# Kernel optimization log

Measured on AMD Instinct MI355X. Metric: run time of the kernel, lower is better.

Reference implementation:

```python
import jax, jax.numpy as jnp
import numpy as np

B, NA, NB = 2, 2048, 2048
DIM_A, DIM_B = 256, 256
HEADS, DH_A, DH_B = 8, 64, 64
INNER_A, INNER_B = DH_A * HEADS, DH_B * HEADS
EPS = 1e-5


def layer_norm(x, w, b):
    m = jnp.mean(x, axis=-1, keepdims=True)
    v = jnp.mean(jnp.square(x - m), axis=-1, keepdims=True)
    return (x - m) * jax.lax.rsqrt(v + EPS) * w + b


def setup_inputs() -> dict:
    key = jax.random.key(0)
    ks = jax.random.split(key, 16)
    s = 0.02
    return {
        "feat_a": jax.random.normal(ks[0], (B, NA, DIM_A), jnp.float32),
        "feat_b": jax.random.normal(ks[1], (B, NB, DIM_B), jnp.float32),
        "mask_a_b": jax.random.bernoulli(ks[2], 0.5, (B, NA, NB)),
        # linear weights stored (in, out)
        "Wq": jax.random.normal(ks[3], (DIM_A, INNER_B), jnp.float32) * s,
        "bq": jnp.zeros((INNER_B,), jnp.float32),
        "Wk": jax.random.normal(ks[4], (DIM_B, INNER_B), jnp.float32) * s,
        "bk": jnp.zeros((INNER_B,), jnp.float32),
        "Wv": jax.random.normal(ks[5], (DIM_B, INNER_A), jnp.float32) * s,
        "bv": jnp.zeros((INNER_A,), jnp.float32),
        "Wg": jax.random.normal(ks[6], (DIM_A, INNER_A), jnp.float32) * s,
        "bg": jnp.zeros((INNER_A,), jnp.float32),
        "Wo": jax.random.normal(ks[7], (INNER_A, DIM_A), jnp.float32) * s,
        "bo": jnp.zeros((DIM_A,), jnp.float32),
        "ln_a_w": jnp.ones((DIM_A,), jnp.float32),
        "ln_a_b": jnp.zeros((DIM_A,), jnp.float32),
        "ln_b_w": jnp.ones((DIM_B,), jnp.float32),
        "ln_b_b": jnp.zeros((DIM_B,), jnp.float32),
        "qln_w": jnp.ones((INNER_B,), jnp.float32),
        "qln_b": jnp.zeros((INNER_B,), jnp.float32),
        "kln_w": jnp.ones((INNER_B,), jnp.float32),
        "kln_b": jnp.zeros((INNER_B,), jnp.float32),
    }


def reference(feat_a, feat_b, mask_a_b, Wq, bq, Wk, bk, Wv, bv, Wg, bg, Wo, bo,
              ln_a_w, ln_a_b, ln_b_w, ln_b_b, qln_w, qln_b, kln_w, kln_b):
    scale = DH_B ** -0.5
    fa = layer_norm(feat_a, ln_a_w, ln_a_b)            # (b, na, dim_a)
    fb = layer_norm(feat_b, ln_b_w, ln_b_b)            # (b, nb, dim_b)
    q = layer_norm(fa @ Wq + bq, qln_w, qln_b)         # (b, na, inner_b)
    k = layer_norm(fb @ Wk + bk, kln_w, kln_b)         # (b, nb, inner_b)
    v = fb @ Wv + bv                                   # (b, nb, inner_a)
    g = fa @ Wg + bg                                   # (b, na, inner_a)
    q = q.reshape(B, NA, HEADS, DH_B)
    k = k.reshape(B, NB, HEADS, DH_B)
    v = v.reshape(B, NB, HEADS, DH_A)
    g = g.reshape(B, NA, HEADS, DH_A)
    sim = jnp.einsum('bihd,bjhd->bhij', q, k) * scale  # (b, h, na, nb)
    neg = jnp.finfo(sim.dtype).min
    sim = jnp.where(mask_a_b[:, None, :, :], sim, neg)
    attn = jax.nn.softmax(sim, axis=-1)
    out = jnp.einsum('bhij,bjhd->bihd', attn, v)       # (b, na, h, dh_a)
    out = jax.nn.sigmoid(g) * out
    out = out.reshape(B, NA, INNER_A)
    return out @ Wo + bo                               # (b, na, dim_a)
```

## Files before the change

kernel.cpp:

```cpp
#include <hip/hip_runtime.h>
#include <hip/hip_bf16.h>

using bf16 = __hip_bfloat16;
typedef short bf16x8 __attribute__((ext_vector_type(8)));
typedef float f32x4 __attribute__((ext_vector_type(4)));
typedef unsigned long long u64;

static constexpr int NA_ = 2048, NB_ = 2048;
static constexpr int H_ = 8, DH_ = 64, INNER_ = 512;
static constexpr int MROWS = 2 * NA_;

__device__ __forceinline__ unsigned short bfbits(float x) {
  bf16 h = __float2bfloat16(x);
  return __builtin_bit_cast(unsigned short, h);
}

__device__ __forceinline__ float exp2_fast(float x) {
#if __has_builtin(__builtin_amdgcn_exp2f)
  return __builtin_amdgcn_exp2f(x);
#else
  return exp2f(x);
#endif
}

__global__ __launch_bounds__(256) void ln_feat_kernel(
    const float* __restrict__ fa_in, const float* __restrict__ fb_in,
    const float* __restrict__ law, const float* __restrict__ lab,
    const float* __restrict__ lbw, const float* __restrict__ lbb,
    bf16* __restrict__ fa, bf16* __restrict__ fb) {
  int row = blockIdx.x;
  const float *src, *w, *bb;
  bf16* dst;
  int r;
  if (row < MROWS) { src = fa_in; w = law; bb = lab; dst = fa; r = row; }
  else             { src = fb_in; w = lbw; bb = lbb; dst = fb; r = row - MROWS; }
  int t = threadIdx.x;
  float x = src[(size_t)r * 256 + t];
  float s = x, s2 = x * x;
#pragma unroll
  for (int m = 32; m >= 1; m >>= 1) { s += __shfl_xor(s, m); s2 += __shfl_xor(s2, m); }
  __shared__ float red[8];
  if ((t & 63) == 0) { red[t >> 6] = s; red[(t >> 6) + 4] = s2; }
  __syncthreads();
  float ts  = red[0] + red[1] + red[2] + red[3];
  float ts2 = red[4] + red[5] + red[6] + red[7];
  float mean = ts * (1.0f / 256.0f);
  float var  = ts2 * (1.0f / 256.0f) - mean * mean;
  float rstd = rsqrtf(var + 1e-5f);
  dst[(size_t)r * 256 + t] = __float2bfloat16((x - mean) * rstd * w[t] + bb[t]);
}

__global__ __launch_bounds__(256) void wconv_kernel(
    const float* __restrict__ Wq, const float* __restrict__ Wk,
    const float* __restrict__ Wv, const float* __restrict__ Wg,
    const float* __restrict__ Wo,
    bf16* __restrict__ Wqgt, bf16* __restrict__ Wkvt,
    bf16* __restrict__ Woth, bf16* __restrict__ Wotl) {
  int z = blockIdx.z;
  int idx = blockIdx.x * 256 + threadIdx.x;
  if (z < 4) {
    const float* W = (z == 0) ? Wq : (z == 1) ? Wk : (z == 2) ? Wv : Wg;
    bf16* Wt = (z == 0 || z == 3) ? Wqgt : Wkvt;
    int half = (z == 2 || z == 3) ? 512 : 0;
    int kk = idx >> 9, n = idx & 511;
    Wt[(half + n) * 256 + kk] = __float2bfloat16(W[idx]);
  } else {
    int kk = idx >> 8, n = idx & 255;
    float w = Wo[idx];
    bf16 hi = __float2bfloat16(w);
    Woth[n * 512 + kk] = hi;
    Wotl[n * 512 + kk] = __float2bfloat16(w - __bfloat162float(hi));
  }
}

__global__ void maskdetect_kernel(const unsigned char* __restrict__ m, int* __restrict__ flag) {
  int t = threadIdx.x;
  if (t == 0) *flag = 0;
  __syncthreads();
  if ((t & 3) != 0 && m[t] != 0) atomicOr(flag, 1);
}

__global__ __launch_bounds__(256) void maskpack_kernel(
    const void* __restrict__ maskp, const int* __restrict__ mflag,
    u64* __restrict__ mbits) {
  const bool m8 = (*mflag != 0);
  int lane = threadIdx.x & 63;
  int wid = threadIdx.x >> 6;
  const size_t NW = 131072;
  for (size_t word = (size_t)blockIdx.x * 4 + wid; word < NW; word += (size_t)gridDim.x * 4) {
    size_t e = word * 64 + lane;
    int v = m8 ? (int)((const unsigned char*)maskp)[e] : ((const int*)maskp)[e];
    u64 bal = __ballot(v != 0);
    if (lane == 0) mbits[word] = bal;
  }
}

template <int VARIANT>
__global__ __launch_bounds__(256) void gemm_fused_kernel(
    const bf16* __restrict__ A, const bf16* __restrict__ Wt,
    const float* __restrict__ bias1, const float* __restrict__ bias2,
    float* __restrict__ C1, bf16* __restrict__ C2) {
  constexpr int K = 256;
  __shared__ __align__(16) bf16 As[64 * 72];
  __shared__ __align__(16) bf16 Bs[64 * 72];
  int n0 = blockIdx.x * 64, m0 = blockIdx.y * 64;
  int t = threadIdx.x, wave = t >> 6, lane = t & 63;
  int lm = lane & 15, quad = lane >> 4, q8 = quad * 8;
  int wm = (wave & 1) * 32, wn = (wave >> 1) * 32;
  f32x4 acc[2][2] = {};
  for (int k0 = 0; k0 < K; k0 += 64) {
    __syncthreads();
#pragma unroll
    for (int i = 0; i < 4; i++) {
      int id = t + 256 * i, r = id >> 4, c = id & 15;
      *(ushort4*)(&As[r * 72 + c * 4]) =
          *(const ushort4*)(A + (size_t)(m0 + r) * K + k0 + c * 4);
      *(ushort4*)(&Bs[r * 72 + c * 4]) =
          *(const ushort4*)(Wt + (size_t)(n0 + r) * K + k0 + c * 4);
    }
    __syncthreads();
#pragma unroll
    for (int kk = 0; kk < 64; kk += 32) {
      bf16x8 af[2], bf_[2];
#pragma unroll
      for (int i = 0; i < 2; i++) {
        af[i]  = *(const bf16x8*)(&As[(wm + i * 16 + lm) * 72 + kk + q8]);
        bf_[i] = *(const bf16x8*)(&Bs[(wn + i * 16 + lm) * 72 + kk + q8]);
      }
#pragma unroll
      for (int mi = 0; mi < 2; mi++)
#pragma unroll
        for (int ni = 0; ni < 2; ni++)
          acc[mi][ni] = __builtin_amdgcn_mfma_f32_16x16x32_bf16(af[mi], bf_[ni], acc[mi][ni], 0, 0, 0);
    }
  }
  if (n0 < 512) {
#pragma unroll
    for (int mi = 0; mi < 2; mi++)
#pragma unroll
      for (int ni = 0; ni < 2; ni++) {
        int n = n0 + wn + ni * 16 + lm;
        float bvv = bias1[n];
        int mb = m0 + wm + mi * 16 + quad * 4;
#pragma unroll
        for (int r = 0; r < 4; r++) C1[(size_t)(mb + r) * 512 + n] = acc[mi][ni][r] + bvv;
      }
  } else if (VARIANT == 0) {
#pragma unroll
    for (int mi = 0; mi < 2; mi++)
#pragma unroll
      for (int ni = 0; ni < 2; ni++) {
        int nn = n0 - 512 + wn + ni * 16 + lm;
        float bvv = bias2[nn];
        int mb = m0 + wm + mi * 16 + quad * 4;
#pragma unroll
        for (int r = 0; r < 4; r++)
          C2[(size_t)(mb + r) * 512 + nn] = __float2bfloat16(acc[mi][ni][r] + bvv);
      }
  } else {
    __syncthreads();
#pragma unroll
    for (int mi = 0; mi < 2; mi++)
#pragma unroll
      for (int ni = 0; ni < 2; ni++) {
        int d_local = wn + ni * 16 + lm;
        float bvv = bias2[n0 - 512 + d_local];
        int j_local = wm + mi * 16 + quad * 4;
#pragma unroll
        for (int r = 0; r < 4; r++)
          As[d_local * 72 + j_local + r] = __float2bfloat16(acc[mi][ni][r] + bvv);
      }
    __syncthreads();
    int bidx = m0 >> 11, j0g = m0 & 2047;
    int hh = (n0 - 512) >> 6;
    int dl = t >> 2, jc = (t & 3) * 16;
    bf16* dstrow = C2 + (size_t)((bidx * 8 + hh) * 64 + dl) * 2048 + j0g + jc;
#pragma unroll
    for (int c = 0; c < 4; c++)
      *(ushort4*)(dstrow + c * 4) = *(const ushort4*)(&As[dl * 72 + jc + c * 4]);
  }
}

__global__ __launch_bounds__(256) void qkln_kernel(
    const float* __restrict__ qpre, const float* __restrict__ kpre,
    const float* __restrict__ qw, const float* __restrict__ qb,
    const float* __restrict__ kw, const float* __restrict__ kb,
    bf16* __restrict__ qo, bf16* __restrict__ ko) {
  int row = blockIdx.x;
  const float *src, *w, *bb;
  bf16* dst;
  int r;
  if (row < MROWS) { src = qpre; w = qw; bb = qb; dst = qo; r = row; }
  else             { src = kpre; w = kw; bb = kb; dst = ko; r = row - MROWS; }
  int t = threadIdx.x;
  float x0 = src[(size_t)r * 512 + t];
  float x1 = src[(size_t)r * 512 + 256 + t];
  float s = x0 + x1, s2 = x0 * x0 + x1 * x1;
#pragma unroll
  for (int m = 32; m >= 1; m >>= 1) { s += __shfl_xor(s, m); s2 += __shfl_xor(s2, m); }
  __shared__ float red[8];
  if ((t & 63) == 0) { red[t >> 6] = s; red[(t >> 6) + 4] = s2; }
  __syncthreads();
  float ts  = red[0] + red[1] + red[2] + red[3];
  float ts2 = red[4] + red[5] + red[6] + red[7];
  float mean = ts * (1.0f / 512.0f);
  float var  = ts2 * (1.0f / 512.0f) - mean * mean;
  float rstd = rsqrtf(var + 1e-5f);
  dst[(size_t)r * 512 + t]       = __float2bfloat16((x0 - mean) * rstd * w[t] + bb[t]);
  dst[(size_t)r * 512 + 256 + t] = __float2bfloat16((x1 - mean) * rstd * w[256 + t] + bb[256 + t]);
}

__global__ __launch_bounds__(512) void attn_kernel(
    const bf16* __restrict__ q, const bf16* __restrict__ k,
    const bf16* __restrict__ vt, const bf16* __restrict__ g,
    const u64* __restrict__ mbits,
    bf16* __restrict__ gh, bf16* __restrict__ gl) {
  __shared__ __align__(16) char smem[65024];
  bf16* Qs = (bf16*)smem;
  bf16* KsB = (bf16*)(smem + 9216);
  bf16* VsB = (bf16*)(smem + 27648);
  bf16* PsB = (bf16*)(smem + 46080);
  float* Om = (float*)(smem + 9216);
  float* Lbuf = (float*)(smem + 64512);

  int qt = blockIdx.x, bh = blockIdx.y;
  int bidx = bh >> 3, h = bh & 7;
  int i0 = qt * 64;
  int t = threadIdx.x, wave = t >> 6, lane = t & 63;
  int jhalf = wave >> 2, w4 = wave & 3;
  int lm = lane & 15, quad = lane >> 4, q8 = quad * 8;
  int lt = t & 255;

#pragma unroll
  for (int i = 0; i < 2; i++) {
    int id = t + 512 * i, r = id >> 4, c = id & 15;
    *(ushort4*)(&Qs[r * 72 + c * 4]) =
        *(const ushort4*)(q + (size_t)(bidx * NA_ + i0 + r) * INNER_ + h * DH_ + c * 4);
  }
  __syncthreads();
  bf16x8 bq[2];
  bq[0] = *(const bf16x8*)(&Qs[(w4 * 16 + lm) * 72 + q8]);
  bq[1] = *(const bf16x8*)(&Qs[(w4 * 16 + lm) * 72 + 32 + q8]);

  f32x4 oacc[4] = {};
  float psum = 0.f;
  const float scale2 = 0.125f * 1.44269504088896f;

  const bf16* kb = k + (size_t)(bidx * NB_) * INNER_ + h * DH_;
  const bf16* vb = vt + (size_t)(bh * DH_) * NB_;
  bf16* Pw = PsB + wave * (16 * 72);
  bf16* Ks = KsB + jhalf * (64 * 72);
  bf16* Vs = VsB + jhalf * (64 * 72);
  const u64* mrp = mbits + ((size_t)(bidx * NA_ + i0 + w4 * 16 + lm)) * (NB_ / 64) + jhalf * 16;

  for (int it = 0; it < 16; it++) {
    int j0 = jhalf * 1024 + it * 64;
    __syncthreads();
#pragma unroll
    for (int i = 0; i < 4; i++) {
      int id = lt + 256 * i, r = id >> 4, c = id & 15;
      *(ushort4*)(&Ks[r * 72 + c * 4]) =
          *(const ushort4*)(kb + (size_t)(j0 + r) * INNER_ + c * 4);
      *(ushort4*)(&Vs[r * 72 + c * 4]) =
          *(const ushort4*)(vb + (size_t)r * NB_ + j0 + c * 4);
    }
    u64 sm = mrp[it] >> (quad * 4);
    __syncthreads();

    f32x4 st[4];
#pragma unroll
    for (int nt = 0; nt < 4; nt++) {
      bf16x8 a0 = *(const bf16x8*)(&Ks[(nt * 16 + lm) * 72 + q8]);
      bf16x8 a1 = *(const bf16x8*)(&Ks[(nt * 16 + lm) * 72 + 32 + q8]);
      f32x4 a = {0.f, 0.f, 0.f, 0.f};
      a = __builtin_amdgcn_mfma_f32_16x16x32_bf16(a0, bq[0], a, 0, 0, 0);
      a = __builtin_amdgcn_mfma_f32_16x16x32_bf16(a1, bq[1], a, 0, 0, 0);
      st[nt] = a;
    }

    float pr[4][4];
#pragma unroll
    for (int nt = 0; nt < 4; nt++)
#pragma unroll
      for (int r = 0; r < 4; r++) {
        float p = exp2_fast(st[nt][r] * scale2 - 16.0f);
        unsigned live = (unsigned)(sm >> (nt * 16 + r)) & 1u;
        pr[nt][r] = live ? p : 0.0f;
      }

    float s0 = (pr[0][0] + pr[0][1]) + (pr[0][2] + pr[0][3]);
    float s1 = (pr[1][0] + pr[1][1]) + (pr[1][2] + pr[1][3]);
    float s2 = (pr[2][0] + pr[2][1]) + (pr[2][2] + pr[2][3]);
    float s3 = (pr[3][0] + pr[3][1]) + (pr[3][2] + pr[3][3]);
    psum += (s0 + s1) + (s2 + s3);

#pragma unroll
    for (int nt = 0; nt < 4; nt++) {
      ushort4 pk;
      pk.x = bfbits(pr[nt][0]);
      pk.y = bfbits(pr[nt][1]);
      pk.z = bfbits(pr[nt][2]);
      pk.w = bfbits(pr[nt][3]);
      *(ushort4*)(Pw + lm * 72 + nt * 16 + quad * 4) = pk;
    }

    bf16x8 ap0 = *(const bf16x8*)(&Pw[lm * 72 + q8]);
    bf16x8 ap1 = *(const bf16x8*)(&Pw[lm * 72 + 32 + q8]);
#pragma unroll
    for (int c = 0; c < 4; c++) {
      bf16x8 v0 = *(const bf16x8*)(&Vs[(c * 16 + lm) * 72 + q8]);
      bf16x8 v1 = *(const bf16x8*)(&Vs[(c * 16 + lm) * 72 + 32 + q8]);
      oacc[c] = __builtin_amdgcn_mfma_f32_16x16x32_bf16(ap0, v0, oacc[c], 0, 0, 0);
      oacc[c] = __builtin_amdgcn_mfma_f32_16x16x32_bf16(ap1, v1, oacc[c], 0, 0, 0);
    }
  }

  psum += __shfl_xor(psum, 16);
  psum += __shfl_xor(psum, 32);

  __syncthreads();
  if (quad == 0) Lbuf[jhalf * 64 + w4 * 16 + lm] = psum;
  if (jhalf == 1) {
#pragma unroll
    for (int c = 0; c < 4; c++)
#pragma unroll
      for (int r = 0; r < 4; r++)
        Om[w4 * (16 * 66) + (quad * 4 + r) * 66 + c * 16 + lm] = oacc[c][r];
  }
  __syncthreads();
  if (jhalf == 0) {
    int mrow = i0 + w4 * 16 + quad * 4;
    float inv[4];
#pragma unroll
    for (int r = 0; r < 4; r++) {
      float l = Lbuf[w4 * 16 + quad * 4 + r] + Lbuf[64 + w4 * 16 + quad * 4 + r];
      inv[r] = 1.0f / l;
    }
#pragma unroll
    for (int c = 0; c < 4; c++) {
      int col = h * DH_ + c * 16 + lm;
#pragma unroll
      for (int r = 0; r < 4; r++) {
        float o = oacc[c][r] + Om[w4 * (16 * 66) + (quad * 4 + r) * 66 + c * 16 + lm];
        size_t idx = (size_t)(bidx * NA_ + mrow + r) * INNER_ + col;
        float gv = __bfloat162float(g[idx]);
        float sig = 1.0f / (1.0f + __expf(-gv));
        float val = o * inv[r] * sig;
        bf16 hi = __float2bfloat16(val);
        gh[idx] = hi;
        gl[idx] = __float2bfloat16(val - __bfloat162float(hi));
      }
    }
  }
}

__global__ __launch_bounds__(256) void gemm_split_kernel(
    const bf16* __restrict__ Ah, const bf16* __restrict__ Al,
    const bf16* __restrict__ Bh, const bf16* __restrict__ Bl,
    const float* __restrict__ bias, float* __restrict__ C,
    int M, int N, int K) {
  __shared__ __align__(16) bf16 Ash[64 * 72];
  __shared__ __align__(16) bf16 Asl[64 * 72];
  __shared__ __align__(16) bf16 Bsh[64 * 72];
  __shared__ __align__(16) bf16 Bsl[64 * 72];
  int n0 = blockIdx.x * 64, m0 = blockIdx.y * 64;
  int t = threadIdx.x, wave = t >> 6, lane = t & 63;
  int lm = lane & 15, quad = lane >> 4, q8 = quad * 8;
  int wm = (wave & 1) * 32, wn = (wave >> 1) * 32;
  f32x4 acc[2][2] = {};
  for (int k0 = 0; k0 < K; k0 += 64) {
    __syncthreads();
#pragma unroll
    for (int i = 0; i < 4; i++) {
      int id = t + 256 * i, r = id >> 4, c = id & 15;
      size_t ga = (size_t)(m0 + r) * K + k0 + c * 4;
      size_t gb = (size_t)(n0 + r) * K + k0 + c * 4;
      *(ushort4*)(&Ash[r * 72 + c * 4]) = *(const ushort4*)(Ah + ga);
      *(ushort4*)(&Asl[r * 72 + c * 4]) = *(const ushort4*)(Al + ga);
      *(ushort4*)(&Bsh[r * 72 + c * 4]) = *(const ushort4*)(Bh + gb);
      *(ushort4*)(&Bsl[r * 72 + c * 4]) = *(const ushort4*)(Bl + gb);
    }
    __syncthreads();
#pragma unroll
    for (int kk = 0; kk < 64; kk += 32) {
      bf16x8 ah[2], al[2], bh[2], bl[2];
#pragma unroll
      for (int i = 0; i < 2; i++) {
        ah[i] = *(const bf16x8*)(&Ash[(wm + i * 16 + lm) * 72 + kk + q8]);
        al[i] = *(const bf16x8*)(&Asl[(wm + i * 16 + lm) * 72 + kk + q8]);
        bh[i] = *(const bf16x8*)(&Bsh[(wn + i * 16 + lm) * 72 + kk + q8]);
        bl[i] = *(const bf16x8*)(&Bsl[(wn + i * 16 + lm) * 72 + kk + q8]);
      }
#pragma unroll
      for (int mi = 0; mi < 2; mi++)
#pragma unroll
        for (int ni = 0; ni < 2; ni++) {
          acc[mi][ni] = __builtin_amdgcn_mfma_f32_16x16x32_bf16(ah[mi], bh[ni], acc[mi][ni], 0, 0, 0);
          acc[mi][ni] = __builtin_amdgcn_mfma_f32_16x16x32_bf16(ah[mi], bl[ni], acc[mi][ni], 0, 0, 0);
          acc[mi][ni] = __builtin_amdgcn_mfma_f32_16x16x32_bf16(al[mi], bh[ni], acc[mi][ni], 0, 0, 0);
        }
    }
  }
#pragma unroll
  for (int mi = 0; mi < 2; mi++)
#pragma unroll
    for (int ni = 0; ni < 2; ni++) {
      int n = n0 + wn + ni * 16 + lm;
      float bvv = bias[n];
      int mb = m0 + wm + mi * 16 + quad * 4;
#pragma unroll
      for (int r = 0; r < 4; r++) C[(size_t)(mb + r) * N + n] = acc[mi][ni][r] + bvv;
    }
}

extern "C" void kernel_launch(void* const* d_in, const int* in_sizes, int n_in,
                              void* d_out, int out_size, void* d_ws, size_t ws_size,
                              hipStream_t stream) {
  const float* feat_a = (const float*)d_in[0];
  const float* feat_b = (const float*)d_in[1];
  const void*  mask   = d_in[2];
  const float* Wq = (const float*)d_in[3];
  const float* bq = (const float*)d_in[4];
  const float* Wk = (const float*)d_in[5];
  const float* bk = (const float*)d_in[6];
  const float* Wv = (const float*)d_in[7];
  const float* bv = (const float*)d_in[8];
  const float* Wg = (const float*)d_in[9];
  const float* bg = (const float*)d_in[10];
  const float* Wo = (const float*)d_in[11];
  const float* bo = (const float*)d_in[12];
  const float* law = (const float*)d_in[13];
  const float* lab = (const float*)d_in[14];
  const float* lbw = (const float*)d_in[15];
  const float* lbb = (const float*)d_in[16];
  const float* qlw = (const float*)d_in[17];
  const float* qlb = (const float*)d_in[18];
  const float* klw = (const float*)d_in[19];
  const float* klb = (const float*)d_in[20];

  char* ws = (char*)d_ws;
  size_t off = 0;
  auto alloc = [&](size_t bytes) -> void* {
    void* p = ws + off;
    off += (bytes + 255) & ~(size_t)255;
    return p;
  };
  bf16* fa    = (bf16*)alloc((size_t)MROWS * 256 * 2);
  bf16* fb    = (bf16*)alloc((size_t)MROWS * 256 * 2);
  bf16* Wqgt  = (bf16*)alloc((size_t)1024 * 256 * 2);
  bf16* Wkvt  = (bf16*)alloc((size_t)1024 * 256 * 2);
  bf16* Woth  = (bf16*)alloc((size_t)131072 * 2);
  bf16* Wotl  = (bf16*)alloc((size_t)131072 * 2);
  float* qpre = (float*)alloc((size_t)MROWS * 512 * 4);
  float* kpre = (float*)alloc((size_t)MROWS * 512 * 4);
  bf16* qb_   = (bf16*)alloc((size_t)MROWS * 512 * 2);
  bf16* kb_   = (bf16*)alloc((size_t)MROWS * 512 * 2);
  bf16* vtb   = (bf16*)alloc((size_t)1024 * 2048 * 2);
  bf16* gbuf  = (bf16*)alloc((size_t)MROWS * 512 * 2);
  bf16* gh    = (bf16*)alloc((size_t)MROWS * 512 * 2);
  bf16* gl    = (bf16*)alloc((size_t)MROWS * 512 * 2);
  u64*  mbits = (u64*)alloc((size_t)131072 * 8);
  int*  mflag = (int*)alloc(256);

  ln_feat_kernel<<<2 * MROWS, 256, 0, stream>>>(feat_a, feat_b, law, lab, lbw, lbb, fa, fb);
  wconv_kernel<<<dim3(512, 1, 5), 256, 0, stream>>>(Wq, Wk, Wv, Wg, Wo, Wqgt, Wkvt, Woth, Wotl);
  maskdetect_kernel<<<1, 256, 0, stream>>>((const unsigned char*)mask, mflag);
  maskpack_kernel<<<2048, 256, 0, stream>>>(mask, mflag, mbits);
  gemm_fused_kernel<0><<<dim3(16, 64), 256, 0, stream>>>(fa, Wqgt, bq, bg, qpre, gbuf);
  gemm_fused_kernel<1><<<dim3(16, 64), 256, 0, stream>>>(fb, Wkvt, bk, bv, kpre, vtb);
  qkln_kernel<<<2 * MROWS, 256, 0, stream>>>(qpre, kpre, qlw, qlb, klw, klb, qb_, kb_);
  attn_kernel<<<dim3(32, 16), 512, 0, stream>>>(qb_, kb_, vtb, gbuf, mbits, gh, gl);
  gemm_split_kernel<<<dim3(4, 64), 256, 0, stream>>>(gh, gl, Woth, Wotl, bo, (float*)d_out, MROWS, 256, 512);
}
```

Baseline: 213.9 us.

## Fuse Q/K projection with LayerNorm and restructure attention and pipeline kernels

Merges the Q/K projection GEMM with its LayerNorm in one kernel, so the fp32 qpre/kpre intermediates and the separate qkln pass go away. G/V projection moves into its own GEMM kernel. The attention kernel now uses 256 threads, each wave covering all key blocks in 128-column tiles, which removes the cross-half partial-output merge through shared memory; it can also use 16x16x16 MFMA with P held in registers. Loads are widened to 16 bytes throughout, the feature LayerNorm packs one row per wave, and the output GEMM uses smaller M tiles for more blocks. The risks are lower occupancy per attention block and longer serial loops per wave.

```diff
diff --git a/kernel.cpp b/kernel.cpp
--- a/kernel.cpp
+++ b/kernel.cpp
@@ -3,24 +3,34 @@
 
 using bf16 = __hip_bfloat16;
 typedef short bf16x8 __attribute__((ext_vector_type(8)));
+typedef short bf16x4 __attribute__((ext_vector_type(4)));
 typedef float f32x4 __attribute__((ext_vector_type(4)));
+typedef unsigned short ushort8_t __attribute__((ext_vector_type(8)));
 typedef unsigned long long u64;
 
 static constexpr int NA_ = 2048, NB_ = 2048;
 static constexpr int H_ = 8, DH_ = 64, INNER_ = 512;
 static constexpr int MROWS = 2 * NA_;
 
+#define MFMA32(a, b, c) __builtin_amdgcn_mfma_f32_16x16x32_bf16(a, b, c, 0, 0, 0)
+
+#if __has_builtin(__builtin_amdgcn_mfma_f32_16x16x16bf16_1k)
+#define HAS_MFMA16 1
+#define MFMA16(a, b, c) __builtin_amdgcn_mfma_f32_16x16x16bf16_1k(a, b, c, 0, 0, 0)
+#elif __has_builtin(__builtin_amdgcn_mfma_f32_16x16x16_bf16)
+#define HAS_MFMA16 1
+#define MFMA16(a, b, c) __builtin_amdgcn_mfma_f32_16x16x16_bf16(a, b, c, 0, 0, 0)
+#else
+#define HAS_MFMA16 0
+#endif
+
 __device__ __forceinline__ unsigned short bfbits(float x) {
   bf16 h = __float2bfloat16(x);
   return __builtin_bit_cast(unsigned short, h);
 }
-
-__device__ __forceinline__ float exp2_fast(float x) {
-#if __has_builtin(__builtin_amdgcn_exp2f)
-  return __builtin_amdgcn_exp2f(x);
-#else
-  return exp2f(x);
-#endif
+__device__ __forceinline__ float b2f(unsigned short u) {
+  unsigned v = ((unsigned)u) << 16;
+  return __builtin_bit_cast(float, v);
 }
 
 __global__ __launch_bounds__(256) void ln_feat_kernel(
@@ -28,42 +38,45 @@
     const float* __restrict__ law, const float* __restrict__ lab,
     const float* __restrict__ lbw, const float* __restrict__ lbb,
     bf16* __restrict__ fa, bf16* __restrict__ fb) {
-  int row = blockIdx.x;
+  int row = blockIdx.x * 4 + (threadIdx.x >> 6);
+  int lane = threadIdx.x & 63;
   const float *src, *w, *bb;
   bf16* dst;
   int r;
   if (row < MROWS) { src = fa_in; w = law; bb = lab; dst = fa; r = row; }
   else             { src = fb_in; w = lbw; bb = lbb; dst = fb; r = row - MROWS; }
-  int t = threadIdx.x;
-  float x = src[(size_t)r * 256 + t];
-  float s = x, s2 = x * x;
+  float4 x = *(const float4*)(src + (size_t)r * 256 + lane * 4);
+  float s  = (x.x + x.y) + (x.z + x.w);
+  float s2 = (x.x * x.x + x.y * x.y) + (x.z * x.z + x.w * x.w);
 #pragma unroll
   for (int m = 32; m >= 1; m >>= 1) { s += __shfl_xor(s, m); s2 += __shfl_xor(s2, m); }
-  __shared__ float red[8];
-  if ((t & 63) == 0) { red[t >> 6] = s; red[(t >> 6) + 4] = s2; }
-  __syncthreads();
-  float ts  = red[0] + red[1] + red[2] + red[3];
-  float ts2 = red[4] + red[5] + red[6] + red[7];
-  float mean = ts * (1.0f / 256.0f);
-  float var  = ts2 * (1.0f / 256.0f) - mean * mean;
+  float mean = s * (1.0f / 256.0f);
+  float var  = s2 * (1.0f / 256.0f) - mean * mean;
   float rstd = rsqrtf(var + 1e-5f);
-  dst[(size_t)r * 256 + t] = __float2bfloat16((x - mean) * rstd * w[t] + bb[t]);
+  float4 wv = *(const float4*)(w + lane * 4);
+  float4 bv = *(const float4*)(bb + lane * 4);
+  ushort4 o;
+  o.x = bfbits((x.x - mean) * rstd * wv.x + bv.x);
+  o.y = bfbits((x.y - mean) * rstd * wv.y + bv.y);
+  o.z = bfbits((x.z - mean) * rstd * wv.z + bv.z);
+  o.w = bfbits((x.w - mean) * rstd * wv.w + bv.w);
+  *(ushort4*)(dst + (size_t)r * 256 + lane * 4) = o;
 }
 
 __global__ __launch_bounds__(256) void wconv_kernel(
     const float* __restrict__ Wq, const float* __restrict__ Wk,
     const float* __restrict__ Wv, const float* __restrict__ Wg,
     const float* __restrict__ Wo,
-    bf16* __restrict__ Wqgt, bf16* __restrict__ Wkvt,
+    bf16* __restrict__ Wqt, bf16* __restrict__ Wkt,
+    bf16* __restrict__ Wvt, bf16* __restrict__ Wgt,
     bf16* __restrict__ Woth, bf16* __restrict__ Wotl) {
   int z = blockIdx.z;
   int idx = blockIdx.x * 256 + threadIdx.x;
   if (z < 4) {
     const float* W = (z == 0) ? Wq : (z == 1) ? Wk : (z == 2) ? Wv : Wg;
-    bf16* Wt = (z == 0 || z == 3) ? Wqgt : Wkvt;
-    int half = (z == 2 || z == 3) ? 512 : 0;
+    bf16* Wt = (z == 0) ? Wqt : (z == 1) ? Wkt : (z == 2) ? Wvt : Wgt;
     int kk = idx >> 9, n = idx & 511;
-    Wt[(half + n) * 256 + kk] = __float2bfloat16(W[idx]);
+    Wt[n * 256 + kk] = __float2bfloat16(W[idx]);
   } else {
     int kk = idx >> 8, n = idx & 255;
     float w = Wo[idx];
@@ -95,14 +108,117 @@
   }
 }
 
-template <int VARIANT>
-__global__ __launch_bounds__(256) void gemm_fused_kernel(
-    const bf16* __restrict__ A, const bf16* __restrict__ Wt,
-    const float* __restrict__ bias1, const float* __restrict__ bias2,
-    float* __restrict__ C1, bf16* __restrict__ C2) {
+__global__ __launch_bounds__(512) void qk_ln_gemm_kernel(
+    const bf16* __restrict__ fa, const bf16* __restrict__ fb,
+    const bf16* __restrict__ Wqt, const bf16* __restrict__ Wkt,
+    const float* __restrict__ bq, const float* __restrict__ bk,
+    const float* __restrict__ qlw, const float* __restrict__ qlb,
+    const float* __restrict__ klw, const float* __restrict__ klb,
+    bf16* __restrict__ qo, bf16* __restrict__ ko) {
+  __shared__ __align__(16) bf16 As[32 * 264];
+  __shared__ float Pred[32 * 16];
+  __shared__ float MV[64];
+  int z = blockIdx.y;
+  const bf16* A    = z ? fb : fa;
+  const bf16* Wt   = z ? Wkt : Wqt;
+  const float* bias = z ? bk : bq;
+  const float* lw  = z ? klw : qlw;
+  const float* lb  = z ? klb : qlb;
+  bf16* out        = z ? ko : qo;
+  int m0 = blockIdx.x * 32;
+  int t = threadIdx.x, wave = t >> 6, lane = t & 63;
+  int lm = lane & 15, quad = lane >> 4, q8 = quad * 8;
+  int n0w = wave * 64;
+#pragma unroll
+  for (int i = 0; i < 2; i++) {
+    int id = t + 512 * i, r = id >> 5, cg = id & 31;
+    *(ushort8_t*)(&As[r * 264 + cg * 8]) =
+        *(const ushort8_t*)(A + (size_t)(m0 + r) * 256 + cg * 8);
+  }
+  __syncthreads();
+  f32x4 acc[2][4] = {};
+  const bf16* wrow[4];
+#pragma unroll
+  for (int ni = 0; ni < 4; ni++) wrow[ni] = Wt + (size_t)(n0w + ni * 16 + lm) * 256;
+#pragma unroll
+  for (int ks = 0; ks < 8; ks++) {
+    int k0 = ks * 32;
+    bf16x8 bf_[4], af[2];
+#pragma unroll
+    for (int ni = 0; ni < 4; ni++) bf_[ni] = *(const bf16x8*)(wrow[ni] + k0 + q8);
+#pragma unroll
+    for (int mi = 0; mi < 2; mi++)
+      af[mi] = *(const bf16x8*)(&As[(mi * 16 + lm) * 264 + k0 + q8]);
+#pragma unroll
+    for (int mi = 0; mi < 2; mi++)
+#pragma unroll
+      for (int ni = 0; ni < 4; ni++)
+        acc[mi][ni] = MFMA32(af[mi], bf_[ni], acc[mi][ni]);
+  }
+  float bv[4];
+#pragma unroll
+  for (int ni = 0; ni < 4; ni++) bv[ni] = bias[n0w + ni * 16 + lm];
+#pragma unroll
+  for (int mi = 0; mi < 2; mi++)
+#pragma unroll
+    for (int ni = 0; ni < 4; ni++)
+#pragma unroll
+      for (int r = 0; r < 4; r++) acc[mi][ni][r] += bv[ni];
+#pragma unroll
+  for (int mi = 0; mi < 2; mi++)
+#pragma unroll
+    for (int r = 0; r < 4; r++) {
+      float s  = (acc[mi][0][r] + acc[mi][1][r]) + (acc[mi][2][r] + acc[mi][3][r]);
+      float s2 = (acc[mi][0][r] * acc[mi][0][r] + acc[mi][1][r] * acc[mi][1][r]) +
+                 (acc[mi][2][r] * acc[mi][2][r] + acc[mi][3][r] * acc[mi][3][r]);
+#pragma unroll
+      for (int m = 1; m <= 8; m <<= 1) { s += __shfl_xor(s, m); s2 += __shfl_xor(s2, m); }
+      if (lm == 0) {
+        int row = mi * 16 + quad * 4 + r;
+        Pred[row * 16 + wave * 2]     = s;
+        Pred[row * 16 + wave * 2 + 1] = s2;
+      }
+    }
+  __syncthreads();
+  if (t < 32) {
+    float s = 0.f, s2 = 0.f;
+#pragma unroll
+    for (int w = 0; w < 8; w++) { s += Pred[t * 16 + w * 2]; s2 += Pred[t * 16 + w * 2 + 1]; }
+    float mean = s * (1.0f / 512.0f);
+    float var  = s2 * (1.0f / 512.0f) - mean * mean;
+    MV[t * 2]     = mean;
+    MV[t * 2 + 1] = rsqrtf(var + 1e-5f);
+  }
+  __syncthreads();
+  float lww[4], lbb_[4];
+#pragma unroll
+  for (int ni = 0; ni < 4; ni++) { lww[ni] = lw[n0w + ni * 16 + lm]; lbb_[ni] = lb[n0w + ni * 16 + lm]; }
+#pragma unroll
+  for (int mi = 0; mi < 2; mi++)
+#pragma unroll
+    for (int r = 0; r < 4; r++) {
+      int row = mi * 16 + quad * 4 + r;
+      float mean = MV[row * 2], rstd = MV[row * 2 + 1];
+      size_t obase = (size_t)(m0 + row) * 512 + n0w;
+#pragma unroll
+      for (int ni = 0; ni < 4; ni++)
+        out[obase + ni * 16 + lm] =
+            __float2bfloat16((acc[mi][ni][r] - mean) * rstd * lww[ni] + lbb_[ni]);
+    }
+}
+
+__global__ __launch_bounds__(256) void gv_gemm_kernel(
+    const bf16* __restrict__ fa, const bf16* __restrict__ fb,
+    const bf16* __restrict__ Wgt, const bf16* __restrict__ Wvt,
+    const float* __restrict__ bg, const float* __restrict__ bv,
+    bf16* __restrict__ gout, bf16* __restrict__ vout) {
   constexpr int K = 256;
   __shared__ __align__(16) bf16 As[64 * 72];
   __shared__ __align__(16) bf16 Bs[64 * 72];
+  int z = blockIdx.z;
+  const bf16* A    = z ? fb : fa;
+  const bf16* Wt   = z ? Wvt : Wgt;
+  const float* bias = z ? bv : bg;
   int n0 = blockIdx.x * 64, m0 = blockIdx.y * 64;
   int t = threadIdx.x, wave = t >> 6, lane = t & 63;
   int lm = lane & 15, quad = lane >> 4, q8 = quad * 8;
@@ -111,12 +227,12 @@
   for (int k0 = 0; k0 < K; k0 += 64) {
     __syncthreads();
 #pragma unroll
-    for (int i = 0; i < 4; i++) {
-      int id = t + 256 * i, r = id >> 4, c = id & 15;
-      *(ushort4*)(&As[r * 72 + c * 4]) =
-          *(const ushort4*)(A + (size_t)(m0 + r) * K + k0 + c * 4);
-      *(ushort4*)(&Bs[r * 72 + c * 4]) =
-          *(const ushort4*)(Wt + (size_t)(n0 + r) * K + k0 + c * 4);
+    for (int i = 0; i < 2; i++) {
+      int id = t + 256 * i, r = id >> 3, cg = id & 7;
+      *(ushort8_t*)(&As[r * 72 + cg * 8]) =
+          *(const ushort8_t*)(A + (size_t)(m0 + r) * K + k0 + cg * 8);
+      *(ushort8_t*)(&Bs[r * 72 + cg * 8]) =
+          *(const ushort8_t*)(Wt + (size_t)(n0 + r) * K + k0 + cg * 8);
     }
     __syncthreads();
 #pragma unroll
@@ -131,31 +247,20 @@
       for (int mi = 0; mi < 2; mi++)
 #pragma unroll
         for (int ni = 0; ni < 2; ni++)
-          acc[mi][ni] = __builtin_amdgcn_mfma_f32_16x16x32_bf16(af[mi], bf_[ni], acc[mi][ni], 0, 0, 0);
-    }
-  }
-  if (n0 < 512) {
+          acc[mi][ni] = MFMA32(af[mi], bf_[ni], acc[mi][ni]);
+    }
+  }
+  if (z == 0) {
 #pragma unroll
     for (int mi = 0; mi < 2; mi++)
 #pragma unroll
       for (int ni = 0; ni < 2; ni++) {
-        int n = n0 + wn + ni * 16 + lm;
-        float bvv = bias1[n];
+        int nn = n0 + wn + ni * 16 + lm;
+        float bvv = bias[nn];
         int mb = m0 + wm + mi * 16 + quad * 4;
 #pragma unroll
-        for (int r = 0; r < 4; r++) C1[(size_t)(mb + r) * 512 + n] = acc[mi][ni][r] + bvv;
-      }
-  } else if (VARIANT == 0) {
-#pragma unroll
-    for (int mi = 0; mi < 2; mi++)
-#pragma unroll
-      for (int ni = 0; ni < 2; ni++) {
-        int nn = n0 - 512 + wn + ni * 16 + lm;
-        float bvv = bias2[nn];
-        int mb = m0 + wm + mi * 16 + quad * 4;
-#pragma unroll
         for (int r = 0; r < 4; r++)
-          C2[(size_t)(mb + r) * 512 + nn] = __float2bfloat16(acc[mi][ni][r] + bvv);
+          gout[(size_t)(mb + r) * 512 + nn] = __float2bfloat16(acc[mi][ni][r] + bvv);
       }
   } else {
     __syncthreads();
@@ -164,7 +269,7 @@
 #pragma unroll
       for (int ni = 0; ni < 2; ni++) {
         int d_local = wn + ni * 16 + lm;
-        float bvv = bias2[n0 - 512 + d_local];
+        float bvv = bias[n0 + d_local];
         int j_local = wm + mi * 16 + quad * 4;
 #pragma unroll
         for (int r = 0; r < 4; r++)
@@ -172,245 +277,204 @@
       }
     __syncthreads();
     int bidx = m0 >> 11, j0g = m0 & 2047;
-    int hh = (n0 - 512) >> 6;
+    int hh = n0 >> 6;
     int dl = t >> 2, jc = (t & 3) * 16;
-    bf16* dstrow = C2 + (size_t)((bidx * 8 + hh) * 64 + dl) * 2048 + j0g + jc;
+    bf16* dstrow = vout + (size_t)((bidx * 8 + hh) * 64 + dl) * 2048 + j0g + jc;
 #pragma unroll
     for (int c = 0; c < 4; c++)
       *(ushort4*)(dstrow + c * 4) = *(const ushort4*)(&As[dl * 72 + jc + c * 4]);
   }
 }
 
-__global__ __launch_bounds__(256) void qkln_kernel(
-    const float* __restrict__ qpre, const float* __restrict__ kpre,
-    const float* __restrict__ qw, const float* __restrict__ qb,
-    const float* __restrict__ kw, const float* __restrict__ kb,
-    bf16* __restrict__ qo, bf16* __restrict__ ko) {
-  int row = blockIdx.x;
-  const float *src, *w, *bb;
-  bf16* dst;
-  int r;
-  if (row < MROWS) { src = qpre; w = qw; bb = qb; dst = qo; r = row; }
-  else             { src = kpre; w = kw; bb = kb; dst = ko; r = row - MROWS; }
-  int t = threadIdx.x;
-  float x0 = src[(size_t)r * 512 + t];
-  float x1 = src[(size_t)r * 512 + 256 + t];
-  float s = x0 + x1, s2 = x0 * x0 + x1 * x1;
-#pragma unroll
-  for (int m = 32; m >= 1; m >>= 1) { s += __shfl_xor(s, m); s2 += __shfl_xor(s2, m); }
-  __shared__ float red[8];
-  if ((t & 63) == 0) { red[t >> 6] = s; red[(t >> 6) + 4] = s2; }
-  __syncthreads();
-  float ts  = red[0] + red[1] + red[2] + red[3];
-  float ts2 = red[4] + red[5] + red[6] + red[7];
-  float mean = ts * (1.0f / 512.0f);
-  float var  = ts2 * (1.0f / 512.0f) - mean * mean;
-  float rstd = rsqrtf(var + 1e-5f);
-  dst[(size_t)r * 512 + t]       = __float2bfloat16((x0 - mean) * rstd * w[t] + bb[t]);
-  dst[(size_t)r * 512 + 256 + t] = __float2bfloat16((x1 - mean) * rstd * w[256 + t] + bb[256 + t]);
-}
-
-__global__ __launch_bounds__(512) void attn_kernel(
+__global__ __launch_bounds__(256) void attn_kernel(
     const bf16* __restrict__ q, const bf16* __restrict__ k,
     const bf16* __restrict__ vt, const bf16* __restrict__ g,
     const u64* __restrict__ mbits,
     bf16* __restrict__ gh, bf16* __restrict__ gl) {
-  __shared__ __align__(16) char smem[65024];
+  __shared__ __align__(16) char smem[45056];
   bf16* Qs = (bf16*)smem;
-  bf16* KsB = (bf16*)(smem + 9216);
-  bf16* VsB = (bf16*)(smem + 27648);
-  bf16* PsB = (bf16*)(smem + 46080);
-  float* Om = (float*)(smem + 9216);
-  float* Lbuf = (float*)(smem + 64512);
-
+  bf16* Ks = (bf16*)(smem + 9216);
+  bf16* Vs = (bf16*)(smem + 27648);
+#if !HAS_MFMA16
+  __shared__ __align__(16) bf16 Ps[4][16 * 136];
+#endif
   int qt = blockIdx.x, bh = blockIdx.y;
   int bidx = bh >> 3, h = bh & 7;
   int i0 = qt * 64;
   int t = threadIdx.x, wave = t >> 6, lane = t & 63;
-  int jhalf = wave >> 2, w4 = wave & 3;
   int lm = lane & 15, quad = lane >> 4, q8 = quad * 8;
-  int lt = t & 255;
 
 #pragma unroll
   for (int i = 0; i < 2; i++) {
-    int id = t + 512 * i, r = id >> 4, c = id & 15;
-    *(ushort4*)(&Qs[r * 72 + c * 4]) =
-        *(const ushort4*)(q + (size_t)(bidx * NA_ + i0 + r) * INNER_ + h * DH_ + c * 4);
+    int id = t + 256 * i, r = id >> 3, cg = id & 7;
+    *(ushort8_t*)(&Qs[r * 72 + cg * 8]) =
+        *(const ushort8_t*)(q + (size_t)(bidx * NA_ + i0 + r) * INNER_ + h * DH_ + cg * 8);
   }
   __syncthreads();
-  bf16x8 bq[2];
-  bq[0] = *(const bf16x8*)(&Qs[(w4 * 16 + lm) * 72 + q8]);
-  bq[1] = *(const bf16x8*)(&Qs[(w4 * 16 + lm) * 72 + 32 + q8]);
-
-  f32x4 oacc[4] = {};
+  bf16x8 bq0 = *(const bf16x8*)(&Qs[(wave * 16 + lm) * 72 + q8]);
+  bf16x8 bq1 = *(const bf16x8*)(&Qs[(wave * 16 + lm) * 72 + 32 + q8]);
+
+  f32x4 oT[4] = {};
   float psum = 0.f;
   const float scale2 = 0.125f * 1.44269504088896f;
 
   const bf16* kb = k + (size_t)(bidx * NB_) * INNER_ + h * DH_;
   const bf16* vb = vt + (size_t)(bh * DH_) * NB_;
-  bf16* Pw = PsB + wave * (16 * 72);
-  bf16* Ks = KsB + jhalf * (64 * 72);
-  bf16* Vs = VsB + jhalf * (64 * 72);
-  const u64* mrp = mbits + ((size_t)(bidx * NA_ + i0 + w4 * 16 + lm)) * (NB_ / 64) + jhalf * 16;
+  const u64* mrp = mbits + (size_t)(bidx * NA_ + i0 + wave * 16 + lm) * (NB_ / 64);
 
   for (int it = 0; it < 16; it++) {
-    int j0 = jhalf * 1024 + it * 64;
+    int j0 = it * 128;
     __syncthreads();
 #pragma unroll
     for (int i = 0; i < 4; i++) {
-      int id = lt + 256 * i, r = id >> 4, c = id & 15;
-      *(ushort4*)(&Ks[r * 72 + c * 4]) =
-          *(const ushort4*)(kb + (size_t)(j0 + r) * INNER_ + c * 4);
-      *(ushort4*)(&Vs[r * 72 + c * 4]) =
-          *(const ushort4*)(vb + (size_t)r * NB_ + j0 + c * 4);
-    }
-    u64 sm = mrp[it] >> (quad * 4);
-    __syncthreads();
-
-    f32x4 st[4];
-#pragma unroll
-    for (int nt = 0; nt < 4; nt++) {
+      int id = t + 256 * i;
+      {
+        int r = id >> 3, cg = id & 7;
+        *(ushort8_t*)(&Ks[r * 72 + cg * 8]) =
+            *(const ushort8_t*)(kb + (size_t)(j0 + r) * INNER_ + cg * 8);
+      }
+      {
+        int d = id >> 4, jg = id & 15;
+        *(ushort8_t*)(&Vs[d * 136 + jg * 8]) =
+            *(const ushort8_t*)(vb + (size_t)d * NB_ + j0 + jg * 8);
+      }
+    }
+    u64 w0 = mrp[it * 2] >> (quad * 4);
+    u64 w1 = mrp[it * 2 + 1] >> (quad * 4);
+    __syncthreads();
+
+    f32x4 st[8];
+#pragma unroll
+    for (int nt = 0; nt < 8; nt++) {
       bf16x8 a0 = *(const bf16x8*)(&Ks[(nt * 16 + lm) * 72 + q8]);
       bf16x8 a1 = *(const bf16x8*)(&Ks[(nt * 16 + lm) * 72 + 32 + q8]);
       f32x4 a = {0.f, 0.f, 0.f, 0.f};
-      a = __builtin_amdgcn_mfma_f32_16x16x32_bf16(a0, bq[0], a, 0, 0, 0);
-      a = __builtin_amdgcn_mfma_f32_16x16x32_bf16(a1, bq[1], a, 0, 0, 0);
+      a = MFMA32(a0, bq0, a);
+      a = MFMA32(a1, bq1, a);
       st[nt] = a;
     }
 
-    float pr[4][4];
-#pragma unroll
-    for (int nt = 0; nt < 4; nt++)
+    bf16x4 pf[8];
+#pragma unroll
+    for (int nt = 0; nt < 8; nt++) {
+      u64 wsel = (nt < 4) ? w0 : w1;
+      int base = (nt & 3) * 16;
 #pragma unroll
       for (int r = 0; r < 4; r++) {
-        float p = exp2_fast(st[nt][r] * scale2 - 16.0f);
-        unsigned live = (unsigned)(sm >> (nt * 16 + r)) & 1u;
-        pr[nt][r] = live ? p : 0.0f;
-      }
-
-    float s0 = (pr[0][0] + pr[0][1]) + (pr[0][2] + pr[0][3]);
-    float s1 = (pr[1][0] + pr[1][1]) + (pr[1][2] + pr[1][3]);
-    float s2 = (pr[2][0] + pr[2][1]) + (pr[2][2] + pr[2][3]);
-    float s3 = (pr[3][0] + pr[3][1]) + (pr[3][2] + pr[3][3]);
-    psum += (s0 + s1) + (s2 + s3);
-
-#pragma unroll
-    for (int nt = 0; nt < 4; nt++) {
-      ushort4 pk;
-      pk.x = bfbits(pr[nt][0]);
-      pk.y = bfbits(pr[nt][1]);
-      pk.z = bfbits(pr[nt][2]);
-      pk.w = bfbits(pr[nt][3]);
-      *(ushort4*)(Pw + lm * 72 + nt * 16 + quad * 4) = pk;
-    }
-
-    bf16x8 ap0 = *(const bf16x8*)(&Pw[lm * 72 + q8]);
-    bf16x8 ap1 = *(const bf16x8*)(&Pw[lm * 72 + 32 + q8]);
-#pragma unroll
-    for (int c = 0; c < 4; c++) {
-      bf16x8 v0 = *(const bf16x8*)(&Vs[(c * 16 + lm) * 72 + q8]);
-      bf16x8 v1 = *(const bf16x8*)(&Vs[(c * 16 + lm) * 72 + 32 + q8]);
-      oacc[c] = __builtin_amdgcn_mfma_f32_16x16x32_bf16(ap0, v0, oacc[c], 0, 0, 0);
-      oacc[c] = __builtin_amdgcn_mfma_f32_16x16x32_bf16(ap1, v1, oacc[c], 0, 0, 0);
-    }
+        float p = exp2f(st[nt][r] * scale2 - 16.0f);
+        unsigned live = (unsigned)(wsel >> (base + r)) & 1u;
+        st[nt][r] = live ? p : 0.0f;
+      }
+      psum += (st[nt][0] + st[nt][1]) + (st[nt][2] + st[nt][3]);
+      bf16x4 pk;
+      pk[0] = (short)bfbits(st[nt][0]);
+      pk[1] = (short)bfbits(st[nt][1]);
+      pk[2] = (short)bfbits(st[nt][2]);
+      pk[3] = (short)bfbits(st[nt][3]);
+      pf[nt] = pk;
+    }
+
+#if HAS_MFMA16
+#pragma unroll
+    for (int nt = 0; nt < 8; nt++) {
+#pragma unroll
+      for (int c = 0; c < 4; c++) {
+        bf16x4 vf = *(const bf16x4*)(&Vs[(c * 16 + lm) * 136 + nt * 16 + quad * 4]);
+        oT[c] = MFMA16(vf, pf[nt], oT[c]);
+      }
+    }
+#else
+#pragma unroll
+    for (int nt = 0; nt < 8; nt++)
+      *(bf16x4*)(&Ps[wave][lm * 136 + nt * 16 + quad * 4]) = pf[nt];
+#pragma unroll
+    for (int kb4 = 0; kb4 < 4; kb4++) {
+      bf16x8 pfr = *(const bf16x8*)(&Ps[wave][lm * 136 + kb4 * 32 + q8]);
+#pragma unroll
+      for (int c = 0; c < 4; c++) {
+        bf16x8 vf = *(const bf16x8*)(&Vs[(c * 16 + lm) * 136 + kb4 * 32 + q8]);
+        oT[c] = MFMA32(vf, pfr, oT[c]);
+      }
+    }
+#endif
   }
 
   psum += __shfl_xor(psum, 16);
   psum += __shfl_xor(psum, 32);
-
-  __syncthreads();
-  if (quad == 0) Lbuf[jhalf * 64 + w4 * 16 + lm] = psum;
-  if (jhalf == 1) {
-#pragma unroll
-    for (int c = 0; c < 4; c++)
-#pragma unroll
-      for (int r = 0; r < 4; r++)
-        Om[w4 * (16 * 66) + (quad * 4 + r) * 66 + c * 16 + lm] = oacc[c][r];
-  }
-  __syncthreads();
-  if (jhalf == 0) {
-    int mrow = i0 + w4 * 16 + quad * 4;
-    float inv[4];
+  float inv = 1.0f / psum;
+
+  size_t gbase = (size_t)(bidx * NA_ + i0 + wave * 16 + lm) * INNER_ + h * DH_;
+#pragma unroll
+  for (int c = 0; c < 4; c++) {
+    int dbase = c * 16 + quad * 4;
+    bf16x4 gv4 = *(const bf16x4*)(g + gbase + dbase);
+    bf16x4 oh, ol;
 #pragma unroll
     for (int r = 0; r < 4; r++) {
-      float l = Lbuf[w4 * 16 + quad * 4 + r] + Lbuf[64 + w4 * 16 + quad * 4 + r];
-      inv[r] = 1.0f / l;
-    }
-#pragma unroll
-    for (int c = 0; c < 4; c++) {
-      int col = h * DH_ + c * 16 + lm;
-#pragma unroll
-      for (int r = 0; r < 4; r++) {
-        float o = oacc[c][r] + Om[w4 * (16 * 66) + (quad * 4 + r) * 66 + c * 16 + lm];
-        size_t idx = (size_t)(bidx * NA_ + mrow + r) * INNER_ + col;
-        float gv = __bfloat162float(g[idx]);
-        float sig = 1.0f / (1.0f + __expf(-gv));
-        float val = o * inv[r] * sig;
-        bf16 hi = __float2bfloat16(val);
-        gh[idx] = hi;
-        gl[idx] = __float2bfloat16(val - __bfloat162float(hi));
-      }
-    }
+      float gvf = b2f((unsigned short)gv4[r]);
+      float sig = 1.0f / (1.0f + __expf(-gvf));
+      float val = oT[c][r] * inv * sig;
+      unsigned short hb = bfbits(val);
+      oh[r] = (short)hb;
+      ol[r] = (short)bfbits(val - b2f(hb));
+    }
+    *(bf16x4*)(gh + gbase + dbase) = oh;
+    *(bf16x4*)(gl + gbase + dbase) = ol;
   }
 }
 
 __global__ __launch_bounds__(256) void gemm_split_kernel(
     const bf16* __restrict__ Ah, const bf16* __restrict__ Al,
     const bf16* __restrict__ Bh, const bf16* __restrict__ Bl,
-    const float* __restrict__ bias, float* __restrict__ C,
-    int M, int N, int K) {
-  __shared__ __align__(16) bf16 Ash[64 * 72];
-  __shared__ __align__(16) bf16 Asl[64 * 72];
+    const float* __restrict__ bias, float* __restrict__ C) {
+  constexpr int K = 512, N = 256;
+  __shared__ __align__(16) bf16 Ash[32 * 72];
+  __shared__ __align__(16) bf16 Asl[32 * 72];
   __shared__ __align__(16) bf16 Bsh[64 * 72];
   __shared__ __align__(16) bf16 Bsl[64 * 72];
-  int n0 = blockIdx.x * 64, m0 = blockIdx.y * 64;
+  int n0 = blockIdx.x * 64, m0 = blockIdx.y * 32;
   int t = threadIdx.x, wave = t >> 6, lane = t & 63;
   int lm = lane & 15, quad = lane >> 4, q8 = quad * 8;
-  int wm = (wave & 1) * 32, wn = (wave >> 1) * 32;
-  f32x4 acc[2][2] = {};
+  int wm = (wave & 1) * 16, wn = (wave >> 1) * 32;
+  f32x4 acc[2] = {};
   for (int k0 = 0; k0 < K; k0 += 64) {
     __syncthreads();
-#pragma unroll
-    for (int i = 0; i < 4; i++) {
-      int id = t + 256 * i, r = id >> 4, c = id & 15;
-      size_t ga = (size_t)(m0 + r) * K + k0 + c * 4;
-      size_t gb = (size_t)(n0 + r) * K + k0 + c * 4;
-      *(ushort4*)(&Ash[r * 72 + c * 4]) = *(const ushort4*)(Ah + ga);
-      *(ushort4*)(&Asl[r * 72 + c * 4]) = *(const ushort4*)(Al + ga);
-      *(ushort4*)(&Bsh[r * 72 + c * 4]) = *(const ushort4*)(Bh + gb);
-      *(ushort4*)(&Bsl[r * 72 + c * 4]) = *(const ushort4*)(Bl + gb);
+    {
+      int r = t >> 3, cg = t & 7;
+      size_t ga = (size_t)(m0 + r) * K + k0 + cg * 8;
+      *(ushort8_t*)(&Ash[r * 72 + cg * 8]) = *(const ushort8_t*)(Ah + ga);
+      *(ushort8_t*)(&Asl[r * 72 + cg * 8]) = *(const ushort8_t*)(Al + ga);
+    }
+#pragma unroll
+    for (int i = 0; i < 2; i++) {
+      int id = t + 256 * i, r = id >> 3, cg = id & 7;
+      size_t gb = (size_t)(n0 + r) * K + k0 + cg * 8;
+      *(ushort8_t*)(&Bsh[r * 72 + cg * 8]) = *(const ushort8_t*)(Bh + gb);
+      *(ushort8_t*)(&Bsl[r * 72 + cg * 8]) = *(const ushort8_t*)(Bl + gb);
     }
     __syncthreads();
 #pragma unroll
     for (int kk = 0; kk < 64; kk += 32) {
-      bf16x8 ah[2], al[2], bh[2], bl[2];
-#pragma unroll
-      for (int i = 0; i < 2; i++) {
-        ah[i] = *(const bf16x8*)(&Ash[(wm + i * 16 + lm) * 72 + kk + q8]);
-        al[i] = *(const bf16x8*)(&Asl[(wm + i * 16 + lm) * 72 + kk + q8]);
-        bh[i] = *(const bf16x8*)(&Bsh[(wn + i * 16 + lm) * 72 + kk + q8]);
-        bl[i] = *(const bf16x8*)(&Bsl[(wn + i * 16 + lm) * 72 + kk + q8]);
-      }
-#pragma unroll
-      for (int mi = 0; mi < 2; mi++)
-#pragma unroll
-        for (int ni = 0; ni < 2; ni++) {
-          acc[mi][ni] = __builtin_amdgcn_mfma_f32_16x16x32_bf16(ah[mi], bh[ni], acc[mi][ni], 0, 0, 0);
-          acc[mi][ni] = __builtin_amdgcn_mfma_f32_16x16x32_bf16(ah[mi], bl[ni], acc[mi][ni], 0, 0, 0);
-          acc[mi][ni] = __builtin_amdgcn_mfma_f32_16x16x32_bf16(al[mi], bh[ni], acc[mi][ni], 0, 0, 0);
-        }
-    }
-  }
-#pragma unroll
-  for (int mi = 0; mi < 2; mi++)
-#pragma unroll
-    for (int ni = 0; ni < 2; ni++) {
-      int n = n0 + wn + ni * 16 + lm;
-      float bvv = bias[n];
-      int mb = m0 + wm + mi * 16 + quad * 4;
-#pragma unroll
-      for (int r = 0; r < 4; r++) C[(size_t)(mb + r) * N + n] = acc[mi][ni][r] + bvv;
-    }
+      bf16x8 ah = *(const bf16x8*)(&Ash[(wm + lm) * 72 + kk + q8]);
+      bf16x8 al = *(const bf16x8*)(&Asl[(wm + lm) * 72 + kk + q8]);
+#pragma unroll
+      for (int ni = 0; ni < 2; ni++) {
+        bf16x8 bh_ = *(const bf16x8*)(&Bsh[(wn + ni * 16 + lm) * 72 + kk + q8]);
+        bf16x8 bl_ = *(const bf16x8*)(&Bsl[(wn + ni * 16 + lm) * 72 + kk + q8]);
+        acc[ni] = MFMA32(ah, bh_, acc[ni]);
+        acc[ni] = MFMA32(ah, bl_, acc[ni]);
+        acc[ni] = MFMA32(al, bh_, acc[ni]);
+      }
+    }
+  }
+#pragma unroll
+  for (int ni = 0; ni < 2; ni++) {
+    int n = n0 + wn + ni * 16 + lm;
+    float bvv = bias[n];
+    int mb = m0 + wm + quad * 4;
+#pragma unroll
+    for (int r = 0; r < 4; r++) C[(size_t)(mb + r) * N + n] = acc[ni][r] + bvv;
+  }
 }
 
 extern "C" void kernel_launch(void* const* d_in, const int* in_sizes, int n_in,
@@ -447,12 +511,12 @@
   };
   bf16* fa    = (bf16*)alloc((size_t)MROWS * 256 * 2);
   bf16* fb    = (bf16*)alloc((size_t)MROWS * 256 * 2);
-  bf16* Wqgt  = (bf16*)alloc((size_t)1024 * 256 * 2);
-  bf16* Wkvt  = (bf16*)alloc((size_t)1024 * 256 * 2);
+  bf16* Wqt   = (bf16*)alloc((size_t)131072 * 2);
+  bf16* Wkt   = (bf16*)alloc((size_t)131072 * 2);
+  bf16* Wvt   = (bf16*)alloc((size_t)131072 * 2);
+  bf16* Wgt   = (bf16*)alloc((size_t)131072 * 2);
   bf16* Woth  = (bf16*)alloc((size_t)131072 * 2);
   bf16* Wotl  = (bf16*)alloc((size_t)131072 * 2);
-  float* qpre = (float*)alloc((size_t)MROWS * 512 * 4);
-  float* kpre = (float*)alloc((size_t)MROWS * 512 * 4);
   bf16* qb_   = (bf16*)alloc((size_t)MROWS * 512 * 2);
   bf16* kb_   = (bf16*)alloc((size_t)MROWS * 512 * 2);
   bf16* vtb   = (bf16*)alloc((size_t)1024 * 2048 * 2);
@@ -462,13 +526,12 @@
   u64*  mbits = (u64*)alloc((size_t)131072 * 8);
   int*  mflag = (int*)alloc(256);
 
-  ln_feat_kernel<<<2 * MROWS, 256, 0, stream>>>(feat_a, feat_b, law, lab, lbw, lbb, fa, fb);
-  wconv_kernel<<<dim3(512, 1, 5), 256, 0, stream>>>(Wq, Wk, Wv, Wg, Wo, Wqgt, Wkvt, Woth, Wotl);
+  ln_feat_kernel<<<2048, 256, 0, stream>>>(feat_a, feat_b, law, lab, lbw, lbb, fa, fb);
+  wconv_kernel<<<dim3(512, 1, 5), 256, 0, stream>>>(Wq, Wk, Wv, Wg, Wo, Wqt, Wkt, Wvt, Wgt, Woth, Wotl);
   maskdetect_kernel<<<1, 256, 0, stream>>>((const unsigned char*)mask, mflag);
   maskpack_kernel<<<2048, 256, 0, stream>>>(mask, mflag, mbits);
-  gemm_fused_kernel<0><<<dim3(16, 64), 256, 0, stream>>>(fa, Wqgt, bq, bg, qpre, gbuf);
-  gemm_fused_kernel<1><<<dim3(16, 64), 256, 0, stream>>>(fb, Wkvt, bk, bv, kpre, vtb);
-  qkln_kernel<<<2 * MROWS, 256, 0, stream>>>(qpre, kpre, qlw, qlb, klw, klb, qb_, kb_);
-  attn_kernel<<<dim3(32, 16), 512, 0, stream>>>(qb_, kb_, vtb, gbuf, mbits, gh, gl);
-  gemm_split_kernel<<<dim3(4, 64), 256, 0, stream>>>(gh, gl, Woth, Wotl, bo, (float*)d_out, MROWS, 256, 512);
-}
+  qk_ln_gemm_kernel<<<dim3(128, 2), 512, 0, stream>>>(fa, fb, Wqt, Wkt, bq, bk, qlw, qlb, klw, klb, qb_, kb_);
+  gv_gemm_kernel<<<dim3(8, 64, 2), 256, 0, stream>>>(fa, fb, Wgt, Wvt, bg, bv, gbuf, vtb);
+  attn_kernel<<<dim3(32, 16), 256, 0, stream>>>(qb_, kb_, vtb, gbuf, mbits, gh, gl);
+  gemm_split_kernel<<<dim3(4, 128), 256, 0, stream>>>(gh, gl, Woth, Wotl, bo, (float*)d_out);
+}
```

Result: slower. 234.5 us (+9.6%).
